# Kernel tuning notes

Hardware: AMD Instinct MI355X
Metric: run time of the kernel (lower is better)

Reference implementation:

```python
import jax, jax.numpy as jnp
import numpy as np

B, S, E = 32, 2048, 1024   # batch, seq_len, embed_dim
R = 512                    # reasoning_dim
STEPS = 8                  # max_reasoning_steps


def setup_inputs() -> dict:
    key = jax.random.key(0)
    ks = jax.random.split(key, 6)
    inv_sqrt_r = 1.0 / np.sqrt(R)
    return {
        "x": jax.random.normal(ks[0], (B, S, E), jnp.float32),
        # BitNetLinear params init: randn * 0.1, zero bias
        "enc_W": jax.random.normal(ks[1], (R, E), jnp.float32) * 0.1,
        "enc_b": jnp.zeros((R,), jnp.float32),
        # nn.LSTM params (uniform(-1/sqrt(R), 1/sqrt(R)) in torch; normal*scale ok for ref)
        "W_ih": jax.random.normal(ks[2], (4 * R, R), jnp.float32) * inv_sqrt_r,
        "W_hh": jax.random.normal(ks[3], (4 * R, R), jnp.float32) * inv_sqrt_r,
        "b_ih": jnp.zeros((4 * R,), jnp.float32),
        "b_hh": jnp.zeros((4 * R,), jnp.float32),
        "dec_W": jax.random.normal(ks[4], (E, R), jnp.float32) * 0.1,
        "dec_b": jnp.zeros((E,), jnp.float32),
        "gate_W": jax.random.normal(ks[5], (1, R), jnp.float32) * 0.1,
        "gate_b": jnp.zeros((1,), jnp.float32),
    }


def bit_linear(x, W, b):
    """Eval-mode BitNetLinear: ternary weights {-1,0,+1}, int8 activations."""
    w_scale = jnp.mean(jnp.abs(W))
    q_w = jnp.sign(W) * (jnp.abs(W) > 0.5 * w_scale).astype(W.dtype)
    i_scale = jnp.max(jnp.abs(x)) / 127.0
    q_x = jnp.clip(jnp.round(x / i_scale), -128.0, 127.0)
    return (q_x @ q_w.T) * w_scale * i_scale + b


def reference(x, enc_W, enc_b, W_ih, W_hh, b_ih, b_hh, dec_W, dec_b, gate_W, gate_b):
    # reasoning_input = encoder(mean over seq)  -> [B, R]
    cur = bit_linear(jnp.mean(x, axis=1), enc_W, enc_b)
    h = jnp.zeros_like(cur)
    c = jnp.zeros_like(cur)
    active = jnp.array(True)  # whether loop is still running (torch break emulation)
    outs, weights = [], []
    for step in range(STEPS):
        gates = cur @ W_ih.T + h @ W_hh.T + (b_ih + b_hh)  # [B, 4R]
        i, f, g, o = jnp.split(gates, 4, axis=-1)          # torch order: i, f, g, o
        c = jax.nn.sigmoid(f) * c + jax.nn.sigmoid(i) * jnp.tanh(g)
        h = jax.nn.sigmoid(o) * jnp.tanh(c)
        outs.append(h)
        weights.append(active)
        gate_score = jax.nn.sigmoid(bit_linear(h, gate_W, gate_b))  # [B, 1]
        trigger = jnp.all(gate_score < 0.5) & (step > 2)
        active = active & jnp.logical_not(trigger)
        cur = h
    outs = jnp.stack(outs, axis=0)                                  # [T, B, R]
    w = jnp.stack(weights, axis=0).astype(x.dtype)                  # [T]
    final = jnp.einsum('t,tbr->br', w, outs) / jnp.sum(w)           # masked mean over steps
    reasoning_out = bit_linear(final, dec_W, dec_b)                 # [B, E]
    return x + reasoning_out[:, None, :]                            # broadcast over seq
```

## Files before the change

### kernel.cpp

```cpp
#include <hip/hip_runtime.h>
#include <math.h>

#define NB 32
#define NS 2048
#define NE 1024
#define NR 512
#define FR 2048
#define NSTEPS 8

#define SCAL   ((size_t)0)
#define PART   ((size_t)1024)
#define WT_IH  (PART + (size_t)NB*32*NE)
#define WT_SUM (WT_IH + (size_t)NR*FR)
#define MEANB  (WT_SUM + (size_t)NR*FR)
#define HBUF   (MEANB + (size_t)NB*NE)
#define CBUF   (HBUF + (size_t)9*NB*NR)
#define FINALB (CBUF + (size_t)NB*NR)
#define ROUTB  (FINALB + (size_t)NB*NR)

__device__ __forceinline__ float sigf(float x){ return 1.0f/(1.0f+expf(-x)); }
__device__ __forceinline__ float quant8(float x, float isc){
    return fminf(fmaxf(rintf(x/isc), -128.0f), 127.0f);
}
__device__ __forceinline__ float tern(float w, float thr){
    return (fabsf(w) > thr) ? (w > 0.0f ? 1.0f : -1.0f) : 0.0f;
}

__global__ __launch_bounds__(256) void k_pre(
    const float4* __restrict__ x4, const float* __restrict__ Wih,
    const float* __restrict__ Whh, const float* __restrict__ encW,
    const float* __restrict__ decW, const float* __restrict__ gateW,
    float* __restrict__ ws)
{
    const int blk = blockIdx.x, tid = threadIdx.x;
    if (blk < 1024) {
        const int b = blk >> 5, ch = blk & 31;
        const float4* xp = x4 + ((size_t)(b*NS + ch*64))*(NE/4) + tid;
        float4 a; a.x=0.f; a.y=0.f; a.z=0.f; a.w=0.f;
        #pragma unroll 4
        for (int i = 0; i < 64; i++) {
            float4 v = xp[(size_t)i*(NE/4)];
            a.x += v.x; a.y += v.y; a.z += v.z; a.w += v.w;
        }
        float4* pp = (float4*)(ws + PART) + (size_t)blk*(NE/4) + tid;
        *pp = a;
    } else if (blk < 1280) {
        const int tt = blk - 1024, jt = tt & 31, kt = tt >> 5;
        const int j0 = jt*64, k0 = kt*64;
        __shared__ float t_ih[64][65];
        __shared__ float t_sm[64][65];
        const int kk = tid & 63, j4 = tid >> 6;
        for (int p = 0; p < 16; p++) {
            int jj = p*4 + j4;
            float a = Wih[(size_t)(j0+jj)*NR + k0 + kk];
            float c = Whh[(size_t)(j0+jj)*NR + k0 + kk];
            t_ih[jj][kk] = a; t_sm[jj][kk] = a + c;
        }
        __syncthreads();
        const int jjj = tid & 63, k4 = tid >> 6;
        for (int p = 0; p < 16; p++) {
            int k2 = p*4 + k4;
            ws[WT_IH  + (size_t)(k0+k2)*FR + j0 + jjj] = t_ih[jjj][k2];
            ws[WT_SUM + (size_t)(k0+k2)*FR + j0 + jjj] = t_sm[jjj][k2];
        }
    } else {
        const float4* w4; int n4; int lb; float* dst;
        if (blk < 1344)      { w4=(const float4*)encW;  n4=NR*NE/4; lb=blk-1280; dst=ws+SCAL+0; }
        else if (blk < 1408) { w4=(const float4*)decW;  n4=NE*NR/4; lb=blk-1344; dst=ws+SCAL+1; }
        else                 { w4=(const float4*)gateW; n4=NR/4;    lb=0;        dst=ws+SCAL+2; }
        float a = 0.f;
        for (int i = lb*256 + tid; i < n4; i += 64*256) {
            float4 v = w4[i];
            a += fabsf(v.x)+fabsf(v.y)+fabsf(v.z)+fabsf(v.w);
        }
        for (int o = 32; o > 0; o >>= 1) a += __shfl_down(a, o, 64);
        __shared__ float lds[4];
        if ((tid & 63) == 0) lds[tid >> 6] = a;
        __syncthreads();
        if (tid == 0) atomicAdd(dst, lds[0]+lds[1]+lds[2]+lds[3]);
    }
}

__global__ __launch_bounds__(256) void k_mean(float* __restrict__ ws)
{
    const int b = blockIdx.x, tid = threadIdx.x;
    const float4* pp = (const float4*)(ws + PART) + (size_t)b*32*(NE/4);
    float4 a; a.x=0.f; a.y=0.f; a.z=0.f; a.w=0.f;
    #pragma unroll 4
    for (int c = 0; c < 32; c++) {
        float4 v = pp[(size_t)c*(NE/4) + tid];
        a.x += v.x; a.y += v.y; a.z += v.z; a.w += v.w;
    }
    const float inv = 1.0f/(float)NS;
    a.x *= inv; a.y *= inv; a.z *= inv; a.w *= inv;
    ((float4*)(ws + MEANB))[(size_t)b*(NE/4) + tid] = a;
    float m = fmaxf(fmaxf(fabsf(a.x), fabsf(a.y)), fmaxf(fabsf(a.z), fabsf(a.w)));
    for (int o = 32; o > 0; o >>= 1) m = fmaxf(m, __shfl_down(m, o, 64));
    __shared__ float lds[4];
    if ((tid & 63) == 0) lds[tid >> 6] = m;
    __syncthreads();
    if (tid == 0) {
        m = fmaxf(fmaxf(lds[0], lds[1]), fmaxf(lds[2], lds[3]));
        atomicMax((unsigned int*)(ws + SCAL + 4), __float_as_uint(m));
    }
}

__global__ __launch_bounds__(256) void k_enc(
    const float* __restrict__ encW, const float* __restrict__ encB,
    float* __restrict__ ws)
{
    const int blk = blockIdx.x, tid = threadIdx.x;
    const int b = blk >> 1;
    const int r = ((blk & 1) << 8) + tid;
    const float wsc = ws[SCAL+0] * (1.0f/(float)(NR*NE));
    const float thr = 0.5f*wsc;
    const float amax = __uint_as_float(((const unsigned int*)(ws + SCAL))[4]);
    const float isc = amax / 127.0f;
    __shared__ float qx[NE];
    const float* mrow = ws + MEANB + (size_t)b*NE;
    for (int e = tid; e < NE; e += 256) qx[e] = quant8(mrow[e], isc);
    __syncthreads();
    const float4* w4 = (const float4*)(encW + (size_t)r*NE);
    float acc = 0.f;
    #pragma unroll 4
    for (int e = 0; e < NE; e += 4) {
        float4 w = w4[e >> 2];
        acc += qx[e  ]*tern(w.x, thr) + qx[e+1]*tern(w.y, thr)
             + qx[e+2]*tern(w.z, thr) + qx[e+3]*tern(w.w, thr);
    }
    ws[HBUF + (size_t)b*NR + r] = acc*wsc*isc + encB[r];
    ws[CBUF + (size_t)b*NR + r] = 0.f;
}

__global__ __launch_bounds__(1024) void k_step(
    const float* __restrict__ wt, const float* __restrict__ bih,
    const float* __restrict__ bhh, float* __restrict__ ws, int t)
{
    const int tid = threadIdx.x, blk = blockIdx.x;
    const int kq = tid >> 8, bi = (tid >> 3) & 31, rl = tid & 7;
    const int r0 = blk*8;
    const float* hprev = ws + HBUF + (size_t)t*NB*NR;
    const float* hrow = hprev + (size_t)bi*NR + kq*128;
    const float* wk = wt + (size_t)(kq*128)*FR + r0 + rl;
    float a0=0.f, a1=0.f, a2=0.f, a3=0.f;
    for (int kk = 0; kk < 128; kk += 4) {
        float4 h4 = *(const float4*)(hrow + kk);
        const float* w0 = wk + (size_t)kk*FR;
        a0 += h4.x*w0[0];        a1 += h4.x*w0[NR];        a2 += h4.x*w0[2*NR];        a3 += h4.x*w0[3*NR];
        a0 += h4.y*w0[FR];       a1 += h4.y*w0[FR+NR];     a2 += h4.y*w0[FR+2*NR];     a3 += h4.y*w0[FR+3*NR];
        a0 += h4.z*w0[2*FR];     a1 += h4.z*w0[2*FR+NR];   a2 += h4.z*w0[2*FR+2*NR];   a3 += h4.z*w0[2*FR+3*NR];
        a0 += h4.w*w0[3*FR];     a1 += h4.w*w0[3*FR+NR];   a2 += h4.w*w0[3*FR+2*NR];   a3 += h4.w*w0[3*FR+3*NR];
    }
    __shared__ float part[4][256][4];
    const int bp = bi*8 + rl;
    part[kq][bp][0]=a0; part[kq][bp][1]=a1; part[kq][bp][2]=a2; part[kq][bp][3]=a3;
    __syncthreads();
    __shared__ float redmax[4];
    float hn = 0.f;
    if (tid < 256) {
        const int bb = tid >> 3, rr = tid & 7;
        const int r = r0 + rr;
        float gi = part[0][tid][0]+part[1][tid][0]+part[2][tid][0]+part[3][tid][0] + (bih[r]        + bhh[r]);
        float gf = part[0][tid][1]+part[1][tid][1]+part[2][tid][1]+part[3][tid][1] + (bih[NR+r]     + bhh[NR+r]);
        float gg = part[0][tid][2]+part[1][tid][2]+part[2][tid][2]+part[3][tid][2] + (bih[2*NR+r]   + bhh[2*NR+r]);
        float go = part[0][tid][3]+part[1][tid][3]+part[2][tid][3]+part[3][tid][3] + (bih[3*NR+r]   + bhh[3*NR+r]);
        float c  = ws[CBUF + (size_t)bb*NR + r];
        float cn = sigf(gf)*c + sigf(gi)*tanhf(gg);
        hn = sigf(go)*tanhf(cn);
        ws[CBUF + (size_t)bb*NR + r] = cn;
        ws[HBUF + (size_t)(t+1)*NB*NR + (size_t)bb*NR + r] = hn;
    }
    float m = fabsf(hn);
    for (int o = 32; o > 0; o >>= 1) m = fmaxf(m, __shfl_down(m, o, 64));
    if (tid < 256 && (tid & 63) == 0) redmax[tid >> 6] = m;
    __syncthreads();
    if (tid == 0) {
        m = fmaxf(fmaxf(redmax[0], redmax[1]), fmaxf(redmax[2], redmax[3]));
        atomicMax((unsigned int*)(ws + SCAL + 8 + t), __float_as_uint(m));
    }
}

__global__ __launch_bounds__(256) void k_gate(
    const float* __restrict__ gateW, const float* __restrict__ gateB,
    float* __restrict__ ws)
{
    const int tid = threadIdx.x;
    __shared__ float qgw[NR];
    __shared__ float lp[256];
    __shared__ float logits[NB];
    __shared__ float red[4];
    const float gwsc = ws[SCAL+2] * (1.0f/(float)NR);
    const float gthr = 0.5f*gwsc;
    for (int i = tid; i < NR; i += 256) qgw[i] = tern(gateW[i], gthr);
    const float gb = gateB[0];
    __syncthreads();
    bool active = true;
    float wts[NSTEPS];
    for (int t = 0; t < NSTEPS; t++) {
        const float amax = __uint_as_float(((const unsigned int*)(ws + SCAL))[8+t]);
        const float isc = amax / 127.0f;
        const float* h = ws + HBUF + (size_t)(t+1)*NB*NR;
        const int b = tid >> 3, ch = tid & 7;
        const float* hb = h + (size_t)b*NR + ch*64;
        float s = 0.f;
        for (int i = 0; i < 64; i++) s += quant8(hb[i], isc) * qgw[ch*64 + i];
        lp[tid] = s;
        __syncthreads();
        if (tid < NB) {
            float z = 0.f;
            for (int c = 0; c < 8; c++) z += lp[tid*8 + c];
            logits[tid] = z*gwsc*isc + gb;
        }
        __syncthreads();
        bool allneg = true;
        for (int bb = 0; bb < NB; bb++)
            allneg = allneg && (sigf(logits[bb]) < 0.5f);
        const bool trigger = allneg && (t > 2);
        wts[t] = active ? 1.0f : 0.0f;
        active = active && !trigger;
        __syncthreads();
    }
    float wsum = 0.f;
    for (int t = 0; t < NSTEPS; t++) wsum += wts[t];
    float m = 0.f;
    for (int i = tid; i < NB*NR; i += 256) {
        float f = 0.f;
        for (int t = 0; t < NSTEPS; t++) f += wts[t]*ws[HBUF + (size_t)(t+1)*NB*NR + i];
        f /= wsum;
        ws[FINALB + i] = f;
        m = fmaxf(m, fabsf(f));
    }
    for (int o = 32; o > 0; o >>= 1) m = fmaxf(m, __shfl_down(m, o, 64));
    if ((tid & 63) == 0) red[tid >> 6] = m;
    __syncthreads();
    if (tid == 0) ws[SCAL+5] = fmaxf(fmaxf(red[0], red[1]), fmaxf(red[2], red[3]));
}

__global__ __launch_bounds__(256) void k_dec(
    const float* __restrict__ decW, const float* __restrict__ decB,
    float* __restrict__ ws)
{
    const int blk = blockIdx.x, tid = threadIdx.x;
    const int b = blk >> 2;
    const int e = ((blk & 3) << 8) + tid;
    const float wsc = ws[SCAL+1] * (1.0f/(float)(NE*NR));
    const float thr = 0.5f*wsc;
    const float isc = ws[SCAL+5] / 127.0f;
    __shared__ float qf[NR];
    const float* frow = ws + FINALB + (size_t)b*NR;
    for (int i = tid; i < NR; i += 256) qf[i] = quant8(frow[i], isc);
    __syncthreads();
    const float4* w4 = (const float4*)(decW + (size_t)e*NR);
    float acc = 0.f;
    #pragma unroll 4
    for (int r = 0; r < NR; r += 4) {
        float4 w = w4[r >> 2];
        acc += qf[r  ]*tern(w.x, thr) + qf[r+1]*tern(w.y, thr)
             + qf[r+2]*tern(w.z, thr) + qf[r+3]*tern(w.w, thr);
    }
    ws[ROUTB + (size_t)b*NE + e] = acc*wsc*isc + decB[e];
}

__global__ __launch_bounds__(256) void k_out(
    const float4* __restrict__ x4, const float* __restrict__ ws,
    float4* __restrict__ out4)
{
    const float4* r4 = (const float4*)(ws + ROUTB);
    const size_t base = (size_t)blockIdx.x*1024 + threadIdx.x;
    #pragma unroll
    for (int i = 0; i < 4; i++) {
        size_t f = base + (size_t)i*256;
        int e4 = (int)(f & 255);
        int b  = (int)(f >> 19);
        float4 xv = x4[f];
        float4 rv = r4[(size_t)b*256 + e4];
        float4 o; o.x = xv.x+rv.x; o.y = xv.y+rv.y; o.z = xv.z+rv.z; o.w = xv.w+rv.w;
        out4[f] = o;
    }
}

extern "C" void kernel_launch(void* const* d_in, const int* in_sizes, int n_in,
                              void* d_out, int out_size, void* d_ws, size_t ws_size,
                              hipStream_t stream)
{
    const float* x     = (const float*)d_in[0];
    const float* encW  = (const float*)d_in[1];
    const float* encB  = (const float*)d_in[2];
    const float* Wih   = (const float*)d_in[3];
    const float* Whh   = (const float*)d_in[4];
    const float* bih   = (const float*)d_in[5];
    const float* bhh   = (const float*)d_in[6];
    const float* decW  = (const float*)d_in[7];
    const float* decB  = (const float*)d_in[8];
    const float* gateW = (const float*)d_in[9];
    const float* gateB = (const float*)d_in[10];
    float* ws  = (float*)d_ws;
    float* out = (float*)d_out;

    hipMemsetAsync(d_ws, 0, 4096, stream);

    hipLaunchKernelGGL(k_pre, dim3(1409), dim3(256), 0, stream,
                       (const float4*)x, Wih, Whh, encW, decW, gateW, ws);
    hipLaunchKernelGGL(k_mean, dim3(32), dim3(256), 0, stream, ws);
    hipLaunchKernelGGL(k_enc, dim3(64), dim3(256), 0, stream, encW, encB, ws);
    for (int t = 0; t < NSTEPS; t++) {
        const float* wt = ws + (t == 0 ? WT_IH : WT_SUM);
        hipLaunchKernelGGL(k_step, dim3(64), dim3(1024), 0, stream, wt, bih, bhh, ws, t);
    }
    hipLaunchKernelGGL(k_gate, dim3(1), dim3(256), 0, stream, gateW, gateB, ws);
    hipLaunchKernelGGL(k_dec, dim3(128), dim3(256), 0, stream, decW, decB, ws);
    hipLaunchKernelGGL(k_out, dim3(16384), dim3(256), 0, stream,
                       (const float4*)x, ws, (float4*)out);
}
```

Baseline: 795.3 us.

## Use bf16 MFMA for LSTM recurrent matmul and parallelize gate/final reduction

```diff
diff --git a/kernel.cpp b/kernel.cpp
--- a/kernel.cpp
+++ b/kernel.cpp
@@ -10,13 +10,18 @@
 
 #define SCAL   ((size_t)0)
 #define PART   ((size_t)1024)
-#define WT_IH  (PART + (size_t)NB*32*NE)
-#define WT_SUM (WT_IH + (size_t)NR*FR)
-#define MEANB  (WT_SUM + (size_t)NR*FR)
+#define WB_IH  (PART + (size_t)NB*32*NE)
+#define WB_SUM (WB_IH + (size_t)FR*NR/2)
+#define MEANB  (WB_SUM + (size_t)FR*NR/2)
 #define HBUF   (MEANB + (size_t)NB*NE)
-#define CBUF   (HBUF + (size_t)9*NB*NR)
+#define HBUFB  (HBUF + (size_t)9*NB*NR)
+#define CBUF   (HBUFB + (size_t)9*NB*NR/2)
 #define FINALB (CBUF + (size_t)NB*NR)
 #define ROUTB  (FINALB + (size_t)NB*NR)
+#define LOGIT  (SCAL + 64)
+
+typedef __attribute__((ext_vector_type(8))) short bf16x8;
+typedef __attribute__((ext_vector_type(4))) float f32x4;
 
 __device__ __forceinline__ float sigf(float x){ return 1.0f/(1.0f+expf(-x)); }
 __device__ __forceinline__ float quant8(float x, float isc){
@@ -24,6 +29,10 @@
 }
 __device__ __forceinline__ float tern(float w, float thr){
     return (fabsf(w) > thr) ? (w > 0.0f ? 1.0f : -1.0f) : 0.0f;
+}
+__device__ __forceinline__ unsigned short f2b(float x){
+    unsigned u = __float_as_uint(x);
+    return (unsigned short)((u + 0x7fffu + ((u >> 16) & 1u)) >> 16);
 }
 
 __global__ __launch_bounds__(256) void k_pre(
@@ -44,29 +53,25 @@
         }
         float4* pp = (float4*)(ws + PART) + (size_t)blk*(NE/4) + tid;
         *pp = a;
-    } else if (blk < 1280) {
-        const int tt = blk - 1024, jt = tt & 31, kt = tt >> 5;
-        const int j0 = jt*64, k0 = kt*64;
-        __shared__ float t_ih[64][65];
-        __shared__ float t_sm[64][65];
-        const int kk = tid & 63, j4 = tid >> 6;
-        for (int p = 0; p < 16; p++) {
-            int jj = p*4 + j4;
-            float a = Wih[(size_t)(j0+jj)*NR + k0 + kk];
-            float c = Whh[(size_t)(j0+jj)*NR + k0 + kk];
-            t_ih[jj][kk] = a; t_sm[jj][kk] = a + c;
-        }
-        __syncthreads();
-        const int jjj = tid & 63, k4 = tid >> 6;
-        for (int p = 0; p < 16; p++) {
-            int k2 = p*4 + k4;
-            ws[WT_IH  + (size_t)(k0+k2)*FR + j0 + jjj] = t_ih[jjj][k2];
-            ws[WT_SUM + (size_t)(k0+k2)*FR + j0 + jjj] = t_sm[jjj][k2];
+    } else if (blk < 1152) {
+        const int lb = blk - 1024;
+        const float4* wih4 = (const float4*)Wih;
+        const float4* whh4 = (const float4*)Whh;
+        ushort4* bi = (ushort4*)(ws + WB_IH);
+        ushort4* bs = (ushort4*)(ws + WB_SUM);
+        #pragma unroll
+        for (int i = 0; i < 8; i++) {
+            const int idx = lb*256 + tid + i*32768;
+            float4 a = wih4[idx];
+            float4 c = whh4[idx];
+            ushort4 va; va.x=f2b(a.x); va.y=f2b(a.y); va.z=f2b(a.z); va.w=f2b(a.w);
+            ushort4 vs; vs.x=f2b(a.x+c.x); vs.y=f2b(a.y+c.y); vs.z=f2b(a.z+c.z); vs.w=f2b(a.w+c.w);
+            bi[idx] = va; bs[idx] = vs;
         }
     } else {
         const float4* w4; int n4; int lb; float* dst;
-        if (blk < 1344)      { w4=(const float4*)encW;  n4=NR*NE/4; lb=blk-1280; dst=ws+SCAL+0; }
-        else if (blk < 1408) { w4=(const float4*)decW;  n4=NE*NR/4; lb=blk-1344; dst=ws+SCAL+1; }
+        if (blk < 1216)      { w4=(const float4*)encW;  n4=NR*NE/4; lb=blk-1152; dst=ws+SCAL+0; }
+        else if (blk < 1280) { w4=(const float4*)decW;  n4=NE*NR/4; lb=blk-1216; dst=ws+SCAL+1; }
         else                 { w4=(const float4*)gateW; n4=NR/4;    lb=0;        dst=ws+SCAL+2; }
         float a = 0.f;
         for (int i = lb*256 + tid; i < n4; i += 64*256) {
@@ -128,112 +133,126 @@
         acc += qx[e  ]*tern(w.x, thr) + qx[e+1]*tern(w.y, thr)
              + qx[e+2]*tern(w.z, thr) + qx[e+3]*tern(w.w, thr);
     }
-    ws[HBUF + (size_t)b*NR + r] = acc*wsc*isc + encB[r];
+    const float h0 = acc*wsc*isc + encB[r];
+    ws[HBUF + (size_t)b*NR + r] = h0;
+    ((unsigned short*)(ws + HBUFB))[(size_t)b*NR + r] = f2b(h0);
     ws[CBUF + (size_t)b*NR + r] = 0.f;
 }
 
-__global__ __launch_bounds__(1024) void k_step(
-    const float* __restrict__ wt, const float* __restrict__ bih,
-    const float* __restrict__ bhh, float* __restrict__ ws, int t)
-{
-    const int tid = threadIdx.x, blk = blockIdx.x;
-    const int kq = tid >> 8, bi = (tid >> 3) & 31, rl = tid & 7;
-    const int r0 = blk*8;
-    const float* hprev = ws + HBUF + (size_t)t*NB*NR;
-    const float* hrow = hprev + (size_t)bi*NR + kq*128;
-    const float* wk = wt + (size_t)(kq*128)*FR + r0 + rl;
-    float a0=0.f, a1=0.f, a2=0.f, a3=0.f;
-    for (int kk = 0; kk < 128; kk += 4) {
-        float4 h4 = *(const float4*)(hrow + kk);
-        const float* w0 = wk + (size_t)kk*FR;
-        a0 += h4.x*w0[0];        a1 += h4.x*w0[NR];        a2 += h4.x*w0[2*NR];        a3 += h4.x*w0[3*NR];
-        a0 += h4.y*w0[FR];       a1 += h4.y*w0[FR+NR];     a2 += h4.y*w0[FR+2*NR];     a3 += h4.y*w0[FR+3*NR];
-        a0 += h4.z*w0[2*FR];     a1 += h4.z*w0[2*FR+NR];   a2 += h4.z*w0[2*FR+2*NR];   a3 += h4.z*w0[2*FR+3*NR];
-        a0 += h4.w*w0[3*FR];     a1 += h4.w*w0[3*FR+NR];   a2 += h4.w*w0[3*FR+2*NR];   a3 += h4.w*w0[3*FR+3*NR];
-    }
-    __shared__ float part[4][256][4];
-    const int bp = bi*8 + rl;
-    part[kq][bp][0]=a0; part[kq][bp][1]=a1; part[kq][bp][2]=a2; part[kq][bp][3]=a3;
-    __syncthreads();
-    __shared__ float redmax[4];
-    float hn = 0.f;
-    if (tid < 256) {
-        const int bb = tid >> 3, rr = tid & 7;
-        const int r = r0 + rr;
-        float gi = part[0][tid][0]+part[1][tid][0]+part[2][tid][0]+part[3][tid][0] + (bih[r]        + bhh[r]);
-        float gf = part[0][tid][1]+part[1][tid][1]+part[2][tid][1]+part[3][tid][1] + (bih[NR+r]     + bhh[NR+r]);
-        float gg = part[0][tid][2]+part[1][tid][2]+part[2][tid][2]+part[3][tid][2] + (bih[2*NR+r]   + bhh[2*NR+r]);
-        float go = part[0][tid][3]+part[1][tid][3]+part[2][tid][3]+part[3][tid][3] + (bih[3*NR+r]   + bhh[3*NR+r]);
-        float c  = ws[CBUF + (size_t)bb*NR + r];
-        float cn = sigf(gf)*c + sigf(gi)*tanhf(gg);
-        hn = sigf(go)*tanhf(cn);
-        ws[CBUF + (size_t)bb*NR + r] = cn;
-        ws[HBUF + (size_t)(t+1)*NB*NR + (size_t)bb*NR + r] = hn;
-    }
+__global__ __launch_bounds__(256) void k_step(
+    const unsigned short* __restrict__ wb,
+    const float* __restrict__ bih, const float* __restrict__ bhh,
+    float* __restrict__ ws, int t)
+{
+    const int tid = threadIdx.x;
+    const int wv = tid >> 6, lane = tid & 63;
+    const int n = lane & 15, quad = lane >> 4;
+    const int mt = blockIdx.x & 1;
+    const int r0 = (blockIdx.x >> 1) << 4;
+    const unsigned short* hb = (const unsigned short*)(ws + HBUFB) + (size_t)t*NB*NR;
+    const unsigned short* ap = hb + (size_t)(mt*16 + n)*NR + quad*8;
+    const unsigned short* bp = wb + (size_t)((wv << 9) + r0 + n)*NR + quad*8;
+    f32x4 acc = {0.f, 0.f, 0.f, 0.f};
+    #pragma unroll
+    for (int k0 = 0; k0 < NR; k0 += 32) {
+        bf16x8 af = *(const bf16x8*)(ap + k0);
+        bf16x8 bf_ = *(const bf16x8*)(bp + k0);
+        acc = __builtin_amdgcn_mfma_f32_16x16x32_bf16(af, bf_, acc, 0, 0, 0);
+    }
+    __shared__ float g[4][16][17];
+    #pragma unroll
+    for (int reg = 0; reg < 4; reg++)
+        g[wv][quad*4 + reg][n] = acc[reg];
+    __syncthreads();
+    const int bl = tid >> 4, rl = tid & 15;
+    const int r = r0 + rl, b = mt*16 + bl;
+    const float gi = g[0][bl][rl] + bih[r]        + bhh[r];
+    const float gf = g[1][bl][rl] + bih[NR+r]     + bhh[NR+r];
+    const float gg = g[2][bl][rl] + bih[2*NR+r]   + bhh[2*NR+r];
+    const float go = g[3][bl][rl] + bih[3*NR+r]   + bhh[3*NR+r];
+    const float c  = ws[CBUF + (size_t)b*NR + r];
+    const float cn = sigf(gf)*c + sigf(gi)*tanhf(gg);
+    const float hn = sigf(go)*tanhf(cn);
+    ws[CBUF + (size_t)b*NR + r] = cn;
+    ws[HBUF + (size_t)(t+1)*NB*NR + (size_t)b*NR + r] = hn;
+    ((unsigned short*)(ws + HBUFB))[(size_t)(t+1)*NB*NR + (size_t)b*NR + r] = f2b(hn);
     float m = fabsf(hn);
     for (int o = 32; o > 0; o >>= 1) m = fmaxf(m, __shfl_down(m, o, 64));
-    if (tid < 256 && (tid & 63) == 0) redmax[tid >> 6] = m;
+    __shared__ float red[4];
+    if (lane == 0) red[wv] = m;
     __syncthreads();
     if (tid == 0) {
-        m = fmaxf(fmaxf(redmax[0], redmax[1]), fmaxf(redmax[2], redmax[3]));
+        m = fmaxf(fmaxf(red[0], red[1]), fmaxf(red[2], red[3]));
         atomicMax((unsigned int*)(ws + SCAL + 8 + t), __float_as_uint(m));
     }
 }
 
-__global__ __launch_bounds__(256) void k_gate(
+__global__ __launch_bounds__(256) void k_glog(
     const float* __restrict__ gateW, const float* __restrict__ gateB,
     float* __restrict__ ws)
 {
-    const int tid = threadIdx.x;
+    const int t = blockIdx.x, tid = threadIdx.x;
     __shared__ float qgw[NR];
     __shared__ float lp[256];
-    __shared__ float logits[NB];
-    __shared__ float red[4];
     const float gwsc = ws[SCAL+2] * (1.0f/(float)NR);
     const float gthr = 0.5f*gwsc;
     for (int i = tid; i < NR; i += 256) qgw[i] = tern(gateW[i], gthr);
-    const float gb = gateB[0];
-    __syncthreads();
+    __syncthreads();
+    const float amax = __uint_as_float(((const unsigned int*)(ws + SCAL))[8 + t]);
+    const float isc = amax / 127.0f;
+    const float* h = ws + HBUF + (size_t)(t+1)*NB*NR;
+    const int b = tid >> 3, ch = tid & 7;
+    const float* hbp = h + (size_t)b*NR + ch*64;
+    float s = 0.f;
+    for (int i = 0; i < 64; i++) s += quant8(hbp[i], isc) * qgw[ch*64 + i];
+    lp[tid] = s;
+    __syncthreads();
+    if (tid < NB) {
+        float z = 0.f;
+        for (int c = 0; c < 8; c++) z += lp[tid*8 + c];
+        ws[LOGIT + t*32 + tid] = z*gwsc*isc + gateB[0];
+    }
+}
+
+__global__ __launch_bounds__(256) void k_final(float* __restrict__ ws)
+{
+    const int tid = threadIdx.x, blk = blockIdx.x;
+    float wts[NSTEPS];
     bool active = true;
-    float wts[NSTEPS];
+    #pragma unroll
     for (int t = 0; t < NSTEPS; t++) {
-        const float amax = __uint_as_float(((const unsigned int*)(ws + SCAL))[8+t]);
-        const float isc = amax / 127.0f;
-        const float* h = ws + HBUF + (size_t)(t+1)*NB*NR;
-        const int b = tid >> 3, ch = tid & 7;
-        const float* hb = h + (size_t)b*NR + ch*64;
-        float s = 0.f;
-        for (int i = 0; i < 64; i++) s += quant8(hb[i], isc) * qgw[ch*64 + i];
-        lp[tid] = s;
-        __syncthreads();
-        if (tid < NB) {
-            float z = 0.f;
-            for (int c = 0; c < 8; c++) z += lp[tid*8 + c];
-            logits[tid] = z*gwsc*isc + gb;
-        }
-        __syncthreads();
         bool allneg = true;
-        for (int bb = 0; bb < NB; bb++)
-            allneg = allneg && (sigf(logits[bb]) < 0.5f);
-        const bool trigger = allneg && (t > 2);
+        for (int b = 0; b < NB; b++)
+            allneg = allneg && (ws[LOGIT + t*32 + b] < 0.0f);
+        const bool trig = allneg && (t > 2);
         wts[t] = active ? 1.0f : 0.0f;
-        active = active && !trigger;
-        __syncthreads();
+        active = active && !trig;
     }
     float wsum = 0.f;
+    #pragma unroll
     for (int t = 0; t < NSTEPS; t++) wsum += wts[t];
+    const float inv = 1.0f/wsum;
     float m = 0.f;
-    for (int i = tid; i < NB*NR; i += 256) {
+    const int i0 = blk*512 + tid;
+    #pragma unroll
+    for (int rep = 0; rep < 2; rep++) {
+        const int i = i0 + rep*256;
         float f = 0.f;
-        for (int t = 0; t < NSTEPS; t++) f += wts[t]*ws[HBUF + (size_t)(t+1)*NB*NR + i];
-        f /= wsum;
+        #pragma unroll
+        for (int t = 0; t < NSTEPS; t++)
+            f += wts[t]*ws[HBUF + (size_t)(t+1)*NB*NR + i];
+        f *= inv;
         ws[FINALB + i] = f;
         m = fmaxf(m, fabsf(f));
     }
     for (int o = 32; o > 0; o >>= 1) m = fmaxf(m, __shfl_down(m, o, 64));
+    __shared__ float red[4];
     if ((tid & 63) == 0) red[tid >> 6] = m;
     __syncthreads();
-    if (tid == 0) ws[SCAL+5] = fmaxf(fmaxf(red[0], red[1]), fmaxf(red[2], red[3]));
+    if (tid == 0) {
+        m = fmaxf(fmaxf(red[0], red[1]), fmaxf(red[2], red[3]));
+        atomicMax((unsigned int*)(ws + SCAL + 5), __float_as_uint(m));
+    }
 }
 
 __global__ __launch_bounds__(256) void k_dec(
@@ -245,7 +264,7 @@
     const int e = ((blk & 3) << 8) + tid;
     const float wsc = ws[SCAL+1] * (1.0f/(float)(NE*NR));
     const float thr = 0.5f*wsc;
-    const float isc = ws[SCAL+5] / 127.0f;
+    const float isc = __uint_as_float(((const unsigned int*)(ws + SCAL))[5]) / 127.0f;
     __shared__ float qf[NR];
     const float* frow = ws + FINALB + (size_t)b*NR;
     for (int i = tid; i < NR; i += 256) qf[i] = quant8(frow[i], isc);
@@ -299,15 +318,17 @@
 
     hipMemsetAsync(d_ws, 0, 4096, stream);
 
-    hipLaunchKernelGGL(k_pre, dim3(1409), dim3(256), 0, stream,
+    hipLaunchKernelGGL(k_pre, dim3(1281), dim3(256), 0, stream,
                        (const float4*)x, Wih, Whh, encW, decW, gateW, ws);
     hipLaunchKernelGGL(k_mean, dim3(32), dim3(256), 0, stream, ws);
     hipLaunchKernelGGL(k_enc, dim3(64), dim3(256), 0, stream, encW, encB, ws);
     for (int t = 0; t < NSTEPS; t++) {
-        const float* wt = ws + (t == 0 ? WT_IH : WT_SUM);
-        hipLaunchKernelGGL(k_step, dim3(64), dim3(1024), 0, stream, wt, bih, bhh, ws, t);
-    }
-    hipLaunchKernelGGL(k_gate, dim3(1), dim3(256), 0, stream, gateW, gateB, ws);
+        const unsigned short* wb =
+            (const unsigned short*)(ws + (t == 0 ? WB_IH : WB_SUM));
+        hipLaunchKernelGGL(k_step, dim3(64), dim3(256), 0, stream, wb, bih, bhh, ws, t);
+    }
+    hipLaunchKernelGGL(k_glog, dim3(8), dim3(256), 0, stream, gateW, gateB, ws);
+    hipLaunchKernelGGL(k_final, dim3(32), dim3(256), 0, stream, ws);
     hipLaunchKernelGGL(k_dec, dim3(128), dim3(256), 0, stream, decW, decB, ws);
     hipLaunchKernelGGL(k_out, dim3(16384), dim3(256), 0, stream,
                        (const float4*)x, ws, (float4*)out);
```

Result: faster. 641.5 us (-19.3%).
